# Kernel optimization log

Measured on AMD Instinct MI355X. Metric: run time of the kernel, lower is better.

The kernel has to match this reference:

```python
import jax, jax.numpy as jnp
import numpy as np

B, M, D, E, N, K = 4, 4096, 768, 1536, 16, 3


def _layernorm(x, g, b, eps=1e-5):
    mu = x.mean(-1, keepdims=True)
    var = ((x - mu) ** 2).mean(-1, keepdims=True)
    return (x - mu) * jax.lax.rsqrt(var + eps) * g + b


def _conv1d(x, w, b):
    # x: (B, E, M), w: (E_out, E_in, K), 'same' padding like Conv1d(padding=k//2)
    p = w.shape[-1] // 2
    y = jax.lax.conv_general_dilated(x, w, window_strides=(1,), padding=[(p, p)],
                                     dimension_numbers=('NCH', 'OIH', 'NCH'))
    return y + b[None, :, None]


def _scan_ssm(xp, A_base, WB, bB, WC, bC, WD, bD, dbias, reverse):
    # xp: (B, M, E); faithful to source: h = (Delta*A_base)*h + (Delta*B)*x, y = sum_n h*C
    if reverse:
        xp = xp[:, ::-1]
    Bp = jnp.einsum('bme,ne->bmn', xp, WB) + bB          # (B, M, N)
    Cp = jnp.einsum('bme,ne->bmn', xp, WC) + bC          # (B, M, N)
    Delta = jax.nn.softplus(jnp.einsum('bme,fe->bmf', xp, WD) + bD + dbias)  # (B, M, E)
    h0 = jnp.zeros((xp.shape[0], A_base.shape[0], A_base.shape[1]), xp.dtype)

    def step(h, inp):
        x_i, d_i, b_i, c_i = inp  # (B,E), (B,E), (B,N), (B,N)
        h = (d_i[..., None] * A_base) * h + (d_i * x_i)[..., None] * b_i[:, None, :]
        return h, jnp.einsum('ben,bn->be', h, c_i)

    xs = tuple(jnp.swapaxes(a, 0, 1) for a in (xp, Delta, Bp, Cp))  # time-major
    _, ys = jax.lax.scan(step, h0, xs)
    y = jnp.swapaxes(ys, 0, 1)  # (B, M, E)
    return y[:, ::-1] if reverse else y


def setup_inputs() -> dict:
    key = jax.random.key(0)
    ks = jax.random.split(key, 16)
    rn = lambda k, shape, s=0.02: jax.random.normal(k, shape, jnp.float32) * s
    return {
        't': jax.random.normal(ks[0], (B, M, D), jnp.float32),
        'ln_g': jnp.ones((D,), jnp.float32), 'ln_b': jnp.zeros((D,), jnp.float32),
        'Wx': rn(ks[1], (E, D)), 'bx': jnp.zeros((E,), jnp.float32),
        'Wz': rn(ks[2], (E, D)), 'bz': jnp.zeros((E,), jnp.float32),
        'Wcf': rn(ks[3], (E, E, K)), 'bcf': jnp.zeros((E,), jnp.float32),
        'Wcb': rn(ks[4], (E, E, K)), 'bcb': jnp.zeros((E,), jnp.float32),
        'WBf': rn(ks[5], (N, E)), 'bBf': jnp.zeros((N,), jnp.float32),
        'WCf': rn(ks[6], (N, E)), 'bCf': jnp.zeros((N,), jnp.float32),
        'WDf': rn(ks[7], (E, E)), 'bDf': jnp.zeros((E,), jnp.float32),
        'WBb': rn(ks[8], (N, E)), 'bBb': jnp.zeros((N,), jnp.float32),
        'WCb': rn(ks[9], (N, E)), 'bCb': jnp.zeros((N,), jnp.float32),
        'WDb': rn(ks[10], (E, E)), 'bDb': jnp.zeros((E,), jnp.float32),
        'Abf': rn(ks[11], (E, N), 0.01), 'Abb': rn(ks[12], (E, N), 0.01),
        'dbf': jnp.zeros((E,), jnp.float32), 'dbb': jnp.zeros((E,), jnp.float32),
        'WT': rn(ks[13], (D, E)), 'bT': jnp.zeros((D,), jnp.float32),
    }


def reference(t, ln_g, ln_b, Wx, bx, Wz, bz, Wcf, bcf, Wcb, bcb,
              WBf, bBf, WCf, bCf, WDf, bDf, WBb, bBb, WCb, bCb, WDb, bDb,
              Abf, Abb, dbf, dbb, WT, bT):
    residual = t
    xn = _layernorm(t, ln_g, ln_b)
    x_proj = xn @ Wx.T + bx        # (B, M, E)
    z = xn @ Wz.T + bz             # (B, M, E)
    xc = jnp.swapaxes(x_proj, 1, 2)
    xp_f = jax.nn.silu(jnp.swapaxes(_conv1d(xc, Wcf, bcf), 1, 2))
    xp_b = jax.nn.silu(jnp.swapaxes(_conv1d(xc, Wcb, bcb), 1, 2))
    y_f = _scan_ssm(xp_f, Abf, WBf, bBf, WCf, bCf, WDf, bDf, dbf, False)
    y_b = _scan_ssm(xp_b, Abb, WBb, bBb, WCb, bCb, WDb, bDb, dbb, True)
    y = (y_f + y_b) * jax.nn.silu(z)
    return y @ WT.T + bT + residual
```

## Files before the change

kernel.cpp:

```cpp
#include <hip/hip_runtime.h>

#define BB 4
#define MM 4096
#define DD 768
#define EE 1536
#define NX 1664
#define BMROWS 16384
#define SCAN_C 128
#define SCAN_W 12

typedef __attribute__((ext_vector_type(8))) short short8;
typedef __attribute__((ext_vector_type(4))) float f32x4;

#define GLD16(src, dst)                                                   \
  __builtin_amdgcn_global_load_lds(                                       \
      (const __attribute__((address_space(1))) void*)(src),               \
      (__attribute__((address_space(3))) void*)(dst), 16, 0, 0)

__device__ __forceinline__ float bf2f(unsigned short u) {
  union { unsigned int i; float f; } v; v.i = ((unsigned int)u) << 16; return v.f;
}
__device__ __forceinline__ unsigned short f2bf(float f) {
  if (f != f) f = 0.f;
  union { float f; unsigned int i; } v; v.f = f;
  unsigned int x = v.i;
  return (unsigned short)((x + 0x7FFFu + ((x >> 16) & 1u)) >> 16);
}
__device__ __forceinline__ float silu_f(float v) { return v / (1.f + __expf(-v)); }
__device__ __forceinline__ float softplus_f(float v) {
  return (v > 15.f) ? v : log1pf(__expf(v));
}

__global__ __launch_bounds__(256) void detect_kernel(const float* __restrict__ t,
                                                     int* __restrict__ flag) {
  __shared__ int cnt[256];
  int c = 0;
  for (int j = 0; j < 256; j++) {
    float v = t[j * 256 + threadIdx.x];
    float a = fabsf(v);
    bool sane = (v == 0.0f) || (a > 9.09e-13f && a < 1.1e12f);
    c += sane ? 1 : 0;
  }
  cnt[threadIdx.x] = c;
  __syncthreads();
  if (threadIdx.x == 0) {
    int s = 0;
    for (int i = 0; i < 256; i++) s += cnt[i];
    flag[0] = (s > 58982) ? 1 : 0;
  }
}

struct NormArgs {
  const void* src[27];
  unsigned short* dst[27];
  int n[27];
  int cb[27];
};

__global__ __launch_bounds__(256) void normalize_all_kernel(NormArgs args,
                                                            const int* __restrict__ flag) {
  const int f = flag[0];
  const int blk = blockIdx.x;
  int t = 0;
#pragma unroll 1
  for (int i = 1; i < 27; ++i)
    if (blk >= args.cb[i]) t = i;
  const void* src = args.src[t];
  unsigned short* dst = args.dst[t];
  const int n = args.n[t];
  const int base = (blk - args.cb[t]) * 1024 + threadIdx.x * 4;
#pragma unroll
  for (int j = 0; j < 4; ++j) {
    const int k = base + j;
    if (k < n)
      dst[k] = f ? f2bf(((const float*)src)[k]) : ((const unsigned short*)src)[k];
  }
}

__global__ __launch_bounds__(256) void zero_kernel(unsigned short* __restrict__ p, int n) {
  const int i = blockIdx.x * 256 + threadIdx.x;
  if (i < n) p[i] = 0;
}

__global__ __launch_bounds__(256) void ln_kernel(
    const unsigned short* __restrict__ t, const unsigned short* __restrict__ gam,
    const unsigned short* __restrict__ bet, unsigned short* __restrict__ xn) {
  const int row = blockIdx.x, tid = threadIdx.x;
  const unsigned short* tr = t + (size_t)row * DD;
  float x0 = bf2f(tr[tid]);
  float x1 = bf2f(tr[tid + 256]);
  float x2 = bf2f(tr[tid + 512]);
  float s = x0 + x1 + x2;
  float s2 = x0 * x0 + x1 * x1 + x2 * x2;
#pragma unroll
  for (int o = 32; o > 0; o >>= 1) {
    s += __shfl_xor(s, o, 64);
    s2 += __shfl_xor(s2, o, 64);
  }
  __shared__ float rs[4], rs2[4];
  if ((tid & 63) == 0) { rs[tid >> 6] = s; rs2[tid >> 6] = s2; }
  __syncthreads();
  float S = rs[0] + rs[1] + rs[2] + rs[3];
  float S2 = rs2[0] + rs2[1] + rs2[2] + rs2[3];
  float mu = S * (1.f / 768.f);
  float var = fmaxf(S2 * (1.f / 768.f) - mu * mu, 0.f);
  float rstd = rsqrtf(var + 1e-5f);
  unsigned short* xo = xn + (size_t)row * DD;
  xo[tid]       = f2bf((x0 - mu) * rstd * bf2f(gam[tid])       + bf2f(bet[tid]));
  xo[tid + 256] = f2bf((x1 - mu) * rstd * bf2f(gam[tid + 256]) + bf2f(bet[tid + 256]));
  xo[tid + 512] = f2bf((x2 - mu) * rstd * bf2f(gam[tid + 512]) + bf2f(bet[tid + 512]));
}

__global__ __launch_bounds__(256) void repack_kernel(
    const void* __restrict__ W, unsigned short* __restrict__ Wk,
    const int* __restrict__ flag) {
  size_t idx = (size_t)blockIdx.x * 256 + threadIdx.x;
  const size_t tot = (size_t)3 * EE * EE;
  if (idx < tot) {
    int i = (int)(idx % EE);
    int rest = (int)(idx / EE);
    int o = rest % EE;
    int k = rest / EE;
    size_t s = ((size_t)o * EE + i) * 3 + k;
    Wk[idx] = flag[0] ? f2bf(((const float*)W)[s]) : ((const unsigned short*)W)[s];
  }
}

template <int EPI, int TAPS>
__global__ __launch_bounds__(256, 3) void gemm_bt(
    const unsigned short* __restrict__ A, const unsigned short* __restrict__ Bw,
    const unsigned short* __restrict__ bias1, const unsigned short* __restrict__ bias2,
    const unsigned short* __restrict__ resid, unsigned short* __restrict__ Cb16,
    float* __restrict__ Cf32, int Mrows, int N, int K,
    const unsigned short* __restrict__ zpad, const int* __restrict__ oflag) {
  __shared__ __align__(16) unsigned short lsA[128 * 64];
  __shared__ __align__(16) unsigned short lsB[128 * 64];
  const int tid = threadIdx.x;
  const int tm = blockIdx.x * 128;
  const int tn = blockIdx.y * 128;
  const int lane = tid & 63;
  const int wave = tid >> 6;
  const int wm = (wave >> 1) * 64, wn = (wave & 1) * 64;
  const int lm = lane & 15, q = lane >> 4;
  const int sr = tid >> 3;
  const int gs = tid & 7;

  f32x4 acc[4][4];
#pragma unroll
  for (int i = 0; i < 4; i++)
#pragma unroll
    for (int j = 0; j < 4; j++) acc[i][j] = (f32x4){0.f, 0.f, 0.f, 0.f};

  int aoff[2][4], boff[2][4];
#pragma unroll
  for (int s = 0; s < 2; s++)
#pragma unroll
    for (int f = 0; f < 4; f++) {
      int m = wm + f * 16 + lm;
      aoff[s][f] = m * 64 + (s * 4 + q) * 8;
      int n = wn + f * 16 + lm;
      boff[s][f] = n * 64 + (s * 4 + q) * 8;
    }

  const int lo = (TAPS == 3) ? (tm / MM) * MM : 0;
  const int hi = lo + MM;

  for (int tap = 0; tap < TAPS; ++tap) {
    const unsigned short* Bt = Bw + (size_t)tap * N * K;
    const int shift = (TAPS == 3) ? (tap - 1) : 0;
    for (int k0 = 0; k0 < K; k0 += 64) {
      const int kc = k0 + gs * 8;
#pragma unroll
      for (int i = 0; i < 4; i++) {
        const int r = i * 32 + sr;
        const unsigned short* ga;
        if (TAPS == 3) {
          const int grow = tm + r + shift;
          const bool ok = (grow >= lo) && (grow < hi);
          ga = ok ? (A + (size_t)grow * K + kc) : (zpad + gs * 8);
        } else {
          ga = A + (size_t)(tm + r) * K + kc;
        }
        GLD16(ga, lsA + r * 64 + gs * 8);
        GLD16(Bt + (size_t)(tn + r) * K + kc, lsB + r * 64 + gs * 8);
      }
      __syncthreads();
#pragma unroll
      for (int s = 0; s < 2; s++) {
        short8 af[4], bfr[4];
#pragma unroll
        for (int f = 0; f < 4; f++) af[f] = *(const short8*)(lsA + aoff[s][f]);
#pragma unroll
        for (int f = 0; f < 4; f++) bfr[f] = *(const short8*)(lsB + boff[s][f]);
#pragma unroll
        for (int i = 0; i < 4; i++)
#pragma unroll
          for (int j = 0; j < 4; j++)
            acc[i][j] = __builtin_amdgcn_mfma_f32_16x16x32_bf16(af[i], bfr[j], acc[i][j], 0, 0, 0);
      }
      __syncthreads();
    }
  }

#pragma unroll
  for (int i = 0; i < 4; i++) {
#pragma unroll
    for (int j = 0; j < 4; j++) {
      int col = tn + wn + j * 16 + lm;
      if (EPI == 4) {
        if (col < EE) {
          float badd = bf2f(bias1[col]) + bf2f(bias2[col]);
#pragma unroll
          for (int r = 0; r < 4; r++) {
            int row = tm + wm + i * 16 + q * 4 + r;
            float v = softplus_f(acc[i][j][r] + badd);
            Cb16[(size_t)row * EE + col] = f2bf(v);
          }
        } else if (col < EE + 32) {
          float badd = bf2f(resid[col - EE]);
#pragma unroll
          for (int r = 0; r < 4; r++) {
            int row = tm + wm + i * 16 + q * 4 + r;
            Cf32[(size_t)row * 32 + (col - EE)] = acc[i][j][r] + badd;
          }
        }
        continue;
      }
      float badd = bf2f(bias1[col]);
      if (EPI == 2) badd += bf2f(bias2[col]);
#pragma unroll
      for (int r = 0; r < 4; r++) {
        int row = tm + wm + i * 16 + q * 4 + r;
        float v = acc[i][j][r] + badd;
        if (EPI == 1) v = silu_f(v);
        if (EPI == 2) v = softplus_f(v);
        const size_t oi = (size_t)row * N + col;
        if (EPI == 3) {
          v += bf2f(resid[oi]);
          if (oflag[0]) Cf32[oi] = (v != v) ? 0.f : v;
          else          Cb16[oi] = f2bf(v);
        } else {
          Cb16[oi] = f2bf(v);
        }
      }
    }
  }
}

__global__ __launch_bounds__(256) void scan_kernel(
    const unsigned short* __restrict__ Delta, const unsigned short* __restrict__ xp,
    const float* __restrict__ BC,
    const unsigned short* __restrict__ Aen, const unsigned short* __restrict__ yprev,
    const unsigned short* __restrict__ sz, unsigned short* __restrict__ yout, int dir) {
  const size_t bo = (size_t)blockIdx.z * MM * EE;
  const size_t bo32 = (size_t)blockIdx.z * MM * 32;
  Delta += bo; xp += bo; yout += bo;
  BC += bo32;
  if (yprev) yprev += bo;
  if (sz) sz += bo;

  const int e = blockIdx.x * 256 + threadIdx.x;
  const int chunk = blockIdx.y;
  const int L = MM / SCAN_C;
  const int p0 = chunk * L;
  const int pw = (chunk == 0) ? 0 : p0 - SCAN_W;
  const int p1 = p0 + L;

  float a[16], h[16];
#pragma unroll
  for (int n = 0; n < 16; n++) {
    a[n] = bf2f(Aen[(size_t)e * 16 + n]);
    h[n] = 0.f;
  }

  int m = dir ? (MM - 1 - pw) : pw;
  float d = bf2f(Delta[(size_t)m * EE + e]);
  float x = bf2f(xp[(size_t)m * EE + e]);
  float bv[16];
  {
    const float4* bp = (const float4*)(BC + (size_t)m * 32);
    *(float4*)&bv[0] = bp[0]; *(float4*)&bv[4] = bp[1];
    *(float4*)&bv[8] = bp[2]; *(float4*)&bv[12] = bp[3];
  }

  for (int p = pw; p < p1; ++p) {
    float dn = 0.f, xnv = 0.f, bn[16];
    if (p + 1 < p1) {
      const int mn = dir ? (MM - 1 - (p + 1)) : (p + 1);
      dn = bf2f(Delta[(size_t)mn * EE + e]);
      xnv = bf2f(xp[(size_t)mn * EE + e]);
      const float4* bp = (const float4*)(BC + (size_t)mn * 32);
      *(float4*)&bn[0] = bp[0]; *(float4*)&bn[4] = bp[1];
      *(float4*)&bn[8] = bp[2]; *(float4*)&bn[12] = bp[3];
    }

    const float dx = d * x;
#pragma unroll
    for (int n = 0; n < 16; n++) h[n] = d * a[n] * h[n] + dx * bv[n];

    if (p >= p0) {
      const int mc = dir ? (MM - 1 - p) : p;
      const float4* cp = (const float4*)(BC + (size_t)mc * 32 + 16);
      float cv[16];
      *(float4*)&cv[0] = cp[0]; *(float4*)&cv[4] = cp[1];
      *(float4*)&cv[8] = cp[2]; *(float4*)&cv[12] = cp[3];
      float y0 = 0.f, y1 = 0.f, y2 = 0.f, y3 = 0.f;
#pragma unroll
      for (int n = 0; n < 16; n += 4) {
        y0 += h[n] * cv[n]; y1 += h[n + 1] * cv[n + 1];
        y2 += h[n + 2] * cv[n + 2]; y3 += h[n + 3] * cv[n + 3];
      }
      const float y = (y0 + y1) + (y2 + y3);
      const size_t idx = (size_t)mc * EE + e;
      if (dir == 0) {
        yout[idx] = f2bf(y);
      } else {
        const float g = (bf2f(yprev[idx]) + y) * bf2f(sz[idx]);
        yout[idx] = f2bf(g);
      }
    }

    d = dn; x = xnv;
#pragma unroll
    for (int n = 0; n < 16; n++) bv[n] = bn[n];
  }
}

extern "C" void kernel_launch(void* const* d_in, const int* in_sizes, int n_in,
                              void* d_out, int out_size, void* d_ws, size_t ws_size,
                              hipStream_t stream) {
  (void)n_in; (void)out_size;

  size_t cur = 0;
  auto alloc_us = [&](size_t n) {
    unsigned short* p = (unsigned short*)d_ws + cur;
    cur += (n + 7) & ~(size_t)7;
    return p;
  };
  int* dflag = (int*)alloc_us(16);
  unsigned short* nt   = alloc_us((size_t)BMROWS * DD);
  unsigned short* xn   = alloc_us((size_t)BMROWS * DD);
  unsigned short* nlng = alloc_us(DD);
  unsigned short* nlnb = alloc_us(DD);
  unsigned short* nWx  = alloc_us((size_t)EE * DD);
  unsigned short* nbx  = alloc_us(EE);
  unsigned short* nWz  = alloc_us((size_t)EE * DD);
  unsigned short* nbz  = alloc_us(EE);
  unsigned short* nbcf = alloc_us(EE);
  unsigned short* nbcb = alloc_us(EE);
  unsigned short* nWDXf = alloc_us((size_t)NX * EE);
  unsigned short* nWDXb = alloc_us((size_t)NX * EE);
  unsigned short* nbDf = alloc_us(EE);
  unsigned short* nbDb = alloc_us(EE);
  unsigned short* nbBCf = alloc_us(32);
  unsigned short* nbBCb = alloc_us(32);
  unsigned short* nAbf = alloc_us((size_t)EE * 16);
  unsigned short* nAbb = alloc_us((size_t)EE * 16);
  unsigned short* ndbf = alloc_us(EE);
  unsigned short* ndbb = alloc_us(EE);
  unsigned short* nWT  = alloc_us((size_t)DD * EE);
  unsigned short* nbT  = alloc_us(DD);
  const size_t WK = (size_t)3 * EE * EE;
  unsigned short* wkF  = alloc_us(WK);
  unsigned short* wkB  = alloc_us(WK);
  unsigned short* zpad = alloc_us(1536);

  const size_t rem_us = (ws_size / 2 > cur) ? (ws_size / 2 - cur) : 0;
  int G = 1;
  {
    const size_t n4 = 5 * (size_t)4 * MM * EE + 4 * (size_t)4 * MM * 32 + 256;
    const size_t n2 = 5 * (size_t)2 * MM * EE + 4 * (size_t)2 * MM * 32 + 256;
    if (n4 <= rem_us) G = 4;
    else if (n2 <= rem_us) G = 2;
  }
  const size_t R = (size_t)G * MM;
  unsigned short* t_xproj = alloc_us(R * EE);
  unsigned short* t_xp    = alloc_us(R * EE);
  unsigned short* t_dlt   = alloc_us(R * EE);
  unsigned short* t_yf    = alloc_us(R * EE);
  unsigned short* t_sz    = alloc_us(R * EE);
  float* BCF = (float*)alloc_us(R * 32 * 2);
  float* BCB = (float*)alloc_us(R * 32 * 2);

  detect_kernel<<<1, 256, 0, stream>>>((const float*)d_in[0], dflag);
  {
    NormArgs na;
    const int idxs[27] = {0, 1, 2, 3, 4, 5, 6, 8, 10, 11, 12, 13, 14, 15, 16,
                          17, 18, 19, 20, 21, 22, 23, 24, 25, 26, 27, 28};
    unsigned short* dsts[27] = {
        nt, nlng, nlnb, nWx, nbx, nWz, nbz, nbcf, nbcb,
        nWDXf + (size_t)1536 * EE,
        nbBCf,
        nWDXf + (size_t)1552 * EE,
        nbBCf + 16,
        nWDXf,
        nbDf,
        nWDXb + (size_t)1536 * EE,
        nbBCb,
        nWDXb + (size_t)1552 * EE,
        nbBCb + 16,
        nWDXb,
        nbDb,
        nAbf, nAbb, ndbf, ndbb, nWT, nbT};
    int cb = 0;
    for (int i = 0; i < 27; ++i) {
      na.src[i] = d_in[idxs[i]];
      na.dst[i] = dsts[i];
      na.n[i] = in_sizes[idxs[i]];
      na.cb[i] = cb;
      cb += (in_sizes[idxs[i]] + 1023) / 1024;
    }
    normalize_all_kernel<<<cb, 256, 0, stream>>>(na, dflag);
  }
  zero_kernel<<<6, 256, 0, stream>>>(zpad, 1536);
  {
    const int zn = 96 * EE;
    zero_kernel<<<(zn + 255) / 256, 256, 0, stream>>>(nWDXf + (size_t)1568 * EE, zn);
    zero_kernel<<<(zn + 255) / 256, 256, 0, stream>>>(nWDXb + (size_t)1568 * EE, zn);
  }
  const int rp_blocks = (int)((WK + 255) / 256);
  repack_kernel<<<rp_blocks, 256, 0, stream>>>(d_in[7], wkF, dflag);
  repack_kernel<<<rp_blocks, 256, 0, stream>>>(d_in[9], wkB, dflag);

  ln_kernel<<<BMROWS, 256, 0, stream>>>(nt, nlng, nlnb, xn);

  const int Mr = (int)R;
  const dim3 gE(Mr / 128, EE / 128);
  const dim3 gX(Mr / 128, NX / 128);
  const dim3 gD(Mr / 128, DD / 128);
  const dim3 gScan(EE / 256, SCAN_C, G);
  const int nGroups = BB / G;

  for (int g = 0; g < nGroups; ++g) {
    const unsigned short* xn_g = xn + (size_t)g * R * DD;
    const unsigned short* nt_g = nt + (size_t)g * R * DD;
    unsigned short* outb_b16 = (unsigned short*)d_out + (size_t)g * R * DD;
    float*          outb_f32 = (float*)d_out + (size_t)g * R * DD;

    gemm_bt<0, 1><<<gE, 256, 0, stream>>>(xn_g, nWx, nbx, nullptr, nullptr,
                                          t_xproj, nullptr, Mr, EE, DD, zpad, dflag);
    gemm_bt<1, 3><<<gE, 256, 0, stream>>>(t_xproj, wkF, nbcf, nullptr, nullptr,
                                          t_xp, nullptr, Mr, EE, EE, zpad, dflag);
    gemm_bt<4, 1><<<gX, 256, 0, stream>>>(t_xp, nWDXf, nbDf, ndbf, nbBCf,
                                          t_dlt, BCF, Mr, NX, EE, zpad, dflag);
    scan_kernel<<<gScan, 256, 0, stream>>>(t_dlt, t_xp, BCF, nAbf,
                                           nullptr, nullptr, t_yf, 0);
    gemm_bt<1, 3><<<gE, 256, 0, stream>>>(t_xproj, wkB, nbcb, nullptr, nullptr,
                                          t_xp, nullptr, Mr, EE, EE, zpad, dflag);
    gemm_bt<4, 1><<<gX, 256, 0, stream>>>(t_xp, nWDXb, nbDb, ndbb, nbBCb,
                                          t_dlt, BCB, Mr, NX, EE, zpad, dflag);
    gemm_bt<1, 1><<<gE, 256, 0, stream>>>(xn_g, nWz, nbz, nullptr, nullptr,
                                          t_sz, nullptr, Mr, EE, DD, zpad, dflag);
    scan_kernel<<<gScan, 256, 0, stream>>>(t_dlt, t_xp, BCB, nAbb,
                                           t_yf, t_sz, t_xproj, 1);
    gemm_bt<3, 1><<<gD, 256, 0, stream>>>(t_xproj, nWT, nbT, nullptr, nt_g,
                                          outb_b16, outb_f32, Mr, DD, EE, zpad, dflag);
  }
}
```

Before: 1.960 ms.

## Reuse A tile across conv taps, read input directly, shrink buffers

```diff
diff --git a/kernel.cpp b/kernel.cpp
--- a/kernel.cpp
+++ b/kernel.cpp
@@ -51,10 +51,10 @@
 }
 
 struct NormArgs {
-  const void* src[27];
-  unsigned short* dst[27];
-  int n[27];
-  int cb[27];
+  const void* src[26];
+  unsigned short* dst[26];
+  int n[26];
+  int cb[26];
 };
 
 __global__ __launch_bounds__(256) void normalize_all_kernel(NormArgs args,
@@ -63,7 +63,7 @@
   const int blk = blockIdx.x;
   int t = 0;
 #pragma unroll 1
-  for (int i = 1; i < 27; ++i)
+  for (int i = 1; i < 26; ++i)
     if (blk >= args.cb[i]) t = i;
   const void* src = args.src[t];
   unsigned short* dst = args.dst[t];
@@ -83,13 +83,19 @@
 }
 
 __global__ __launch_bounds__(256) void ln_kernel(
-    const unsigned short* __restrict__ t, const unsigned short* __restrict__ gam,
-    const unsigned short* __restrict__ bet, unsigned short* __restrict__ xn) {
+    const void* __restrict__ t, const unsigned short* __restrict__ gam,
+    const unsigned short* __restrict__ bet, unsigned short* __restrict__ xn,
+    const int* __restrict__ flag) {
   const int row = blockIdx.x, tid = threadIdx.x;
-  const unsigned short* tr = t + (size_t)row * DD;
-  float x0 = bf2f(tr[tid]);
-  float x1 = bf2f(tr[tid + 256]);
-  float x2 = bf2f(tr[tid + 512]);
+  const int f = flag[0];
+  float x0, x1, x2;
+  if (f) {
+    const float* tr = (const float*)t + (size_t)row * DD;
+    x0 = tr[tid]; x1 = tr[tid + 256]; x2 = tr[tid + 512];
+  } else {
+    const unsigned short* tr = (const unsigned short*)t + (size_t)row * DD;
+    x0 = bf2f(tr[tid]); x1 = bf2f(tr[tid + 256]); x2 = bf2f(tr[tid + 512]);
+  }
   float s = x0 + x1 + x2;
   float s2 = x0 * x0 + x1 * x1 + x2 * x2;
 #pragma unroll
@@ -127,13 +133,14 @@
 }
 
 template <int EPI, int TAPS>
-__global__ __launch_bounds__(256, 3) void gemm_bt(
+__global__ __launch_bounds__(256, 4) void gemm_bt(
     const unsigned short* __restrict__ A, const unsigned short* __restrict__ Bw,
     const unsigned short* __restrict__ bias1, const unsigned short* __restrict__ bias2,
-    const unsigned short* __restrict__ resid, unsigned short* __restrict__ Cb16,
-    float* __restrict__ Cf32, int Mrows, int N, int K,
+    const unsigned short* __restrict__ resid16, const float* __restrict__ residf,
+    unsigned short* __restrict__ Cb16, float* __restrict__ Cf32,
+    int Mrows, int N, int K,
     const unsigned short* __restrict__ zpad, const int* __restrict__ oflag) {
-  __shared__ __align__(16) unsigned short lsA[128 * 64];
+  __shared__ __align__(16) unsigned short lsA[130 * 64];
   __shared__ __align__(16) unsigned short lsB[128 * 64];
   const int tid = threadIdx.x;
   const int tm = blockIdx.x * 128;
@@ -162,27 +169,70 @@
       boff[s][f] = n * 64 + (s * 4 + q) * 8;
     }
 
-  const int lo = (TAPS == 3) ? (tm / MM) * MM : 0;
-  const int hi = lo + MM;
-
-  for (int tap = 0; tap < TAPS; ++tap) {
-    const unsigned short* Bt = Bw + (size_t)tap * N * K;
-    const int shift = (TAPS == 3) ? (tap - 1) : 0;
+  const short8 zero8 = (short8){0, 0, 0, 0, 0, 0, 0, 0};
+
+  if (TAPS == 3) {
+    const int lo = (tm / MM) * MM;
+    const int hi = lo + MM;
     for (int k0 = 0; k0 < K; k0 += 64) {
       const int kc = k0 + gs * 8;
 #pragma unroll
       for (int i = 0; i < 4; i++) {
         const int r = i * 32 + sr;
-        const unsigned short* ga;
-        if (TAPS == 3) {
-          const int grow = tm + r + shift;
-          const bool ok = (grow >= lo) && (grow < hi);
-          ga = ok ? (A + (size_t)grow * K + kc) : (zpad + gs * 8);
-        } else {
-          ga = A + (size_t)(tm + r) * K + kc;
+        GLD16(A + (size_t)(tm + r) * K + kc, lsA + (r + 1) * 64 + gs * 8);
+      }
+      if (tid < 16) {
+        const int hs = tid >> 3;
+        const int ch = tid & 7;
+        const int grow = hs ? (tm + 128) : (tm - 1);
+        const bool ok = (grow >= lo) && (grow < hi);
+        const short8 v = ok ? *(const short8*)(A + (size_t)grow * K + k0 + ch * 8)
+                            : zero8;
+        *(short8*)(lsA + (hs ? 129 : 0) * 64 + ch * 8) = v;
+      }
+#pragma unroll
+      for (int i = 0; i < 4; i++) {
+        const int r = i * 32 + sr;
+        GLD16(Bw + (size_t)(tn + r) * K + kc, lsB + r * 64 + gs * 8);
+      }
+      __syncthreads();
+#pragma unroll
+      for (int tap = 0; tap < 3; ++tap) {
+#pragma unroll
+        for (int s = 0; s < 2; s++) {
+          short8 af[4], bfr[4];
+#pragma unroll
+          for (int f = 0; f < 4; f++)
+            af[f] = *(const short8*)(lsA + aoff[s][f] + tap * 64);
+#pragma unroll
+          for (int f = 0; f < 4; f++) bfr[f] = *(const short8*)(lsB + boff[s][f]);
+#pragma unroll
+          for (int i = 0; i < 4; i++)
+#pragma unroll
+            for (int j = 0; j < 4; j++)
+              acc[i][j] = __builtin_amdgcn_mfma_f32_16x16x32_bf16(af[i], bfr[j], acc[i][j], 0, 0, 0);
         }
-        GLD16(ga, lsA + r * 64 + gs * 8);
-        GLD16(Bt + (size_t)(tn + r) * K + kc, lsB + r * 64 + gs * 8);
+        if (tap < 2) {
+          __syncthreads();
+          const unsigned short* Bt = Bw + (size_t)(tap + 1) * N * K;
+#pragma unroll
+          for (int i = 0; i < 4; i++) {
+            const int r = i * 32 + sr;
+            GLD16(Bt + (size_t)(tn + r) * K + kc, lsB + r * 64 + gs * 8);
+          }
+          __syncthreads();
+        }
+      }
+      __syncthreads();
+    }
+  } else {
+    for (int k0 = 0; k0 < K; k0 += 64) {
+      const int kc = k0 + gs * 8;
+#pragma unroll
+      for (int i = 0; i < 4; i++) {
+        const int r = i * 32 + sr;
+        GLD16(A + (size_t)(tm + r) * K + kc, lsA + r * 64 + gs * 8);
+        GLD16(Bw + (size_t)(tn + r) * K + kc, lsB + r * 64 + gs * 8);
       }
       __syncthreads();
 #pragma unroll
@@ -217,7 +267,7 @@
             Cb16[(size_t)row * EE + col] = f2bf(v);
           }
         } else if (col < EE + 32) {
-          float badd = bf2f(resid[col - EE]);
+          float badd = bf2f(resid16[col - EE]);
 #pragma unroll
           for (int r = 0; r < 4; r++) {
             int row = tm + wm + i * 16 + q * 4 + r;
@@ -236,9 +286,10 @@
         if (EPI == 2) v = softplus_f(v);
         const size_t oi = (size_t)row * N + col;
         if (EPI == 3) {
-          v += bf2f(resid[oi]);
-          if (oflag[0]) Cf32[oi] = (v != v) ? 0.f : v;
-          else          Cb16[oi] = f2bf(v);
+          const int f = oflag[0];
+          v += f ? residf[oi] : bf2f(resid16[oi]);
+          if (f) Cf32[oi] = (v != v) ? 0.f : v;
+          else   Cb16[oi] = f2bf(v);
         } else {
           Cb16[oi] = f2bf(v);
         }
@@ -251,7 +302,7 @@
     const unsigned short* __restrict__ Delta, const unsigned short* __restrict__ xp,
     const float* __restrict__ BC,
     const unsigned short* __restrict__ Aen, const unsigned short* __restrict__ yprev,
-    const unsigned short* __restrict__ sz, unsigned short* __restrict__ yout, int dir) {
+    const unsigned short* sz, unsigned short* yout, int dir) {
   const size_t bo = (size_t)blockIdx.z * MM * EE;
   const size_t bo32 = (size_t)blockIdx.z * MM * 32;
   Delta += bo; xp += bo; yout += bo;
@@ -338,7 +389,6 @@
     return p;
   };
   int* dflag = (int*)alloc_us(16);
-  unsigned short* nt   = alloc_us((size_t)BMROWS * DD);
   unsigned short* xn   = alloc_us((size_t)BMROWS * DD);
   unsigned short* nlng = alloc_us(DD);
   unsigned short* nlnb = alloc_us(DD);
@@ -365,30 +415,30 @@
   unsigned short* wkB  = alloc_us(WK);
   unsigned short* zpad = alloc_us(1536);
 
-  const size_t rem_us = (ws_size / 2 > cur) ? (ws_size / 2 - cur) : 0;
+  const size_t avail = (ws_size / 2 > cur) ? (ws_size / 2 - cur) : 0;
   int G = 1;
   {
-    const size_t n4 = 5 * (size_t)4 * MM * EE + 4 * (size_t)4 * MM * 32 + 256;
-    const size_t n2 = 5 * (size_t)2 * MM * EE + 4 * (size_t)2 * MM * 32 + 256;
-    if (n4 <= rem_us) G = 4;
-    else if (n2 <= rem_us) G = 2;
+    auto need = [&](int g) {
+      return (size_t)4 * ((size_t)g * MM * EE) + 2 * ((size_t)g * MM * 64) + 1024;
+    };
+    if (need(4) <= avail) G = 4;
+    else if (need(2) <= avail) G = 2;
   }
   const size_t R = (size_t)G * MM;
-  unsigned short* t_xproj = alloc_us(R * EE);
-  unsigned short* t_xp    = alloc_us(R * EE);
-  unsigned short* t_dlt   = alloc_us(R * EE);
-  unsigned short* t_yf    = alloc_us(R * EE);
-  unsigned short* t_sz    = alloc_us(R * EE);
-  float* BCF = (float*)alloc_us(R * 32 * 2);
-  float* BCB = (float*)alloc_us(R * 32 * 2);
+  unsigned short* U1 = alloc_us(R * EE);
+  unsigned short* U2 = alloc_us(R * EE);
+  unsigned short* U3 = alloc_us(R * EE);
+  unsigned short* U4 = alloc_us(R * EE);
+  float* BCF = (float*)alloc_us(R * 64);
+  float* BCB = (float*)alloc_us(R * 64);
 
   detect_kernel<<<1, 256, 0, stream>>>((const float*)d_in[0], dflag);
   {
     NormArgs na;
-    const int idxs[27] = {0, 1, 2, 3, 4, 5, 6, 8, 10, 11, 12, 13, 14, 15, 16,
+    const int idxs[26] = {1, 2, 3, 4, 5, 6, 8, 10, 11, 12, 13, 14, 15, 16,
                           17, 18, 19, 20, 21, 22, 23, 24, 25, 26, 27, 28};
-    unsigned short* dsts[27] = {
-        nt, nlng, nlnb, nWx, nbx, nWz, nbz, nbcf, nbcb,
+    unsigned short* dsts[26] = {
+        nlng, nlnb, nWx, nbx, nWz, nbz, nbcf, nbcb,
         nWDXf + (size_t)1536 * EE,
         nbBCf,
         nWDXf + (size_t)1552 * EE,
@@ -403,7 +453,7 @@
         nbDb,
         nAbf, nAbb, ndbf, ndbb, nWT, nbT};
     int cb = 0;
-    for (int i = 0; i < 27; ++i) {
+    for (int i = 0; i < 26; ++i) {
       na.src[i] = d_in[idxs[i]];
       na.dst[i] = dsts[i];
       na.n[i] = in_sizes[idxs[i]];
@@ -422,7 +472,7 @@
   repack_kernel<<<rp_blocks, 256, 0, stream>>>(d_in[7], wkF, dflag);
   repack_kernel<<<rp_blocks, 256, 0, stream>>>(d_in[9], wkB, dflag);
 
-  ln_kernel<<<BMROWS, 256, 0, stream>>>(nt, nlng, nlnb, xn);
+  ln_kernel<<<BMROWS, 256, 0, stream>>>(d_in[0], nlng, nlnb, xn, dflag);
 
   const int Mr = (int)R;
   const dim3 gE(Mr / 128, EE / 128);
@@ -433,27 +483,28 @@
 
   for (int g = 0; g < nGroups; ++g) {
     const unsigned short* xn_g = xn + (size_t)g * R * DD;
-    const unsigned short* nt_g = nt + (size_t)g * R * DD;
+    const unsigned short* res16 = (const unsigned short*)d_in[0] + (size_t)g * R * DD;
+    const float*          res32 = (const float*)d_in[0] + (size_t)g * R * DD;
     unsigned short* outb_b16 = (unsigned short*)d_out + (size_t)g * R * DD;
     float*          outb_f32 = (float*)d_out + (size_t)g * R * DD;
 
-    gemm_bt<0, 1><<<gE, 256, 0, stream>>>(xn_g, nWx, nbx, nullptr, nullptr,
-                                          t_xproj, nullptr, Mr, EE, DD, zpad, dflag);
-    gemm_bt<1, 3><<<gE, 256, 0, stream>>>(t_xproj, wkF, nbcf, nullptr, nullptr,
-                                          t_xp, nullptr, Mr, EE, EE, zpad, dflag);
-    gemm_bt<4, 1><<<gX, 256, 0, stream>>>(t_xp, nWDXf, nbDf, ndbf, nbBCf,
-                                          t_dlt, BCF, Mr, NX, EE, zpad, dflag);
-    scan_kernel<<<gScan, 256, 0, stream>>>(t_dlt, t_xp, BCF, nAbf,
-                                           nullptr, nullptr, t_yf, 0);
-    gemm_bt<1, 3><<<gE, 256, 0, stream>>>(t_xproj, wkB, nbcb, nullptr, nullptr,
-                                          t_xp, nullptr, Mr, EE, EE, zpad, dflag);
-    gemm_bt<4, 1><<<gX, 256, 0, stream>>>(t_xp, nWDXb, nbDb, ndbb, nbBCb,
-                                          t_dlt, BCB, Mr, NX, EE, zpad, dflag);
-    gemm_bt<1, 1><<<gE, 256, 0, stream>>>(xn_g, nWz, nbz, nullptr, nullptr,
-                                          t_sz, nullptr, Mr, EE, DD, zpad, dflag);
-    scan_kernel<<<gScan, 256, 0, stream>>>(t_dlt, t_xp, BCB, nAbb,
-                                           t_yf, t_sz, t_xproj, 1);
-    gemm_bt<3, 1><<<gD, 256, 0, stream>>>(t_xproj, nWT, nbT, nullptr, nt_g,
+    gemm_bt<0, 1><<<gE, 256, 0, stream>>>(xn_g, nWx, nbx, nullptr, nullptr, nullptr,
+                                          U1, nullptr, Mr, EE, DD, zpad, dflag);
+    gemm_bt<1, 3><<<gE, 256, 0, stream>>>(U1, wkF, nbcf, nullptr, nullptr, nullptr,
+                                          U2, nullptr, Mr, EE, EE, zpad, dflag);
+    gemm_bt<4, 1><<<gX, 256, 0, stream>>>(U2, nWDXf, nbDf, ndbf, nbBCf, nullptr,
+                                          U3, BCF, Mr, NX, EE, zpad, dflag);
+    scan_kernel<<<gScan, 256, 0, stream>>>(U3, U2, BCF, nAbf,
+                                           nullptr, nullptr, U4, 0);
+    gemm_bt<1, 3><<<gE, 256, 0, stream>>>(U1, wkB, nbcb, nullptr, nullptr, nullptr,
+                                          U3, nullptr, Mr, EE, EE, zpad, dflag);
+    gemm_bt<4, 1><<<gX, 256, 0, stream>>>(U3, nWDXb, nbDb, ndbb, nbBCb, nullptr,
+                                          U1, BCB, Mr, NX, EE, zpad, dflag);
+    gemm_bt<1, 1><<<gE, 256, 0, stream>>>(xn_g, nWz, nbz, nullptr, nullptr, nullptr,
+                                          U2, nullptr, Mr, EE, DD, zpad, dflag);
+    scan_kernel<<<gScan, 256, 0, stream>>>(U1, U3, BCB, nAbb,
+                                           U4, U2, U2, 1);
+    gemm_bt<3, 1><<<gD, 256, 0, stream>>>(U2, nWT, nbT, nullptr, res16, res32,
                                           outb_b16, outb_f32, Mr, DD, EE, zpad, dflag);
   }
 }
```

Result: faster. 1.688 ms (-13.9%).
